# Performance work log

Measured on AMD Instinct MI355X. Metric: run time of the kernel, lower is better.

## Reference

```python
import jax, jax.numpy as jnp
import numpy as np

N, E, D, H, L = 100000, 800000, 64, 2, 2
C = D  # out_channels per head
NEG_SLOPE = 0.2


def setup_inputs() -> dict:
    key = jax.random.key(0)
    ks = jax.random.split(key, 10)
    x = jax.random.normal(ks[0], (N, D), dtype=jnp.float32)
    # random edges with no self loops (PyG GATv2 removes then re-adds self loops)
    src = jax.random.randint(ks[1], (E,), 0, N, dtype=jnp.int64)
    off = jax.random.randint(ks[2], (E,), 1, N, dtype=jnp.int64)
    dst = (src + off) % N
    edges_connectivity = jnp.stack([src, dst], axis=0)
    s = 1.0 / np.sqrt(D)
    Wl = jax.random.normal(ks[3], (L, D, H * C), dtype=jnp.float32) * s
    bl = jnp.zeros((L, H * C), dtype=jnp.float32)
    Wr = jax.random.normal(ks[4], (L, D, H * C), dtype=jnp.float32) * s
    br = jnp.zeros((L, H * C), dtype=jnp.float32)
    att = jax.random.normal(ks[5], (L, H, C), dtype=jnp.float32) * s
    bias = jnp.zeros((L, C), dtype=jnp.float32)
    return {"embeded_nodes_features": x, "edges_connectivity": edges_connectivity,
            "Wl": Wl, "bl": bl, "Wr": Wr, "br": br, "att": att, "bias": bias}


def _gatv2_layer(x, src, dst, Wl, bl, Wr, br, att, bias):
    # x: [N, D]; src/dst: [E'] (self loops already appended)
    xl = (x @ Wl + bl).reshape(N, H, C)
    xr = (x @ Wr + br).reshape(N, H, C)
    z = xl[src] + xr[dst]                                  # [E', H, C]
    e = jnp.einsum('ehc,hc->eh', jax.nn.leaky_relu(z, NEG_SLOPE), att)
    m = jax.ops.segment_max(e, dst, num_segments=N)        # [N, H]
    a = jnp.exp(e - m[dst])
    denom = jax.ops.segment_sum(a, dst, num_segments=N)    # [N, H]
    alpha = a / (denom[dst] + 1e-16)
    out = jax.ops.segment_sum(alpha[:, :, None] * xl[src], dst, num_segments=N)
    return out.mean(axis=1) + bias                         # concat=False -> mean over heads


def reference(embeded_nodes_features, edges_connectivity, Wl, bl, Wr, br, att, bias):
    loop = jnp.arange(N, dtype=edges_connectivity.dtype)
    src = jnp.concatenate([edges_connectivity[0], loop])
    dst = jnp.concatenate([edges_connectivity[1], loop])
    x = embeded_nodes_features  # dropout p=0 -> no-op
    for i in range(L):
        x = _gatv2_layer(x, src, dst, Wl[i], bl[i], Wr[i], br[i], att[i], bias[i])
        if i < L - 1:
            x = jax.nn.gelu(x)
    return x
```

## Files before the change

### kernel.cpp

```cpp
#include <hip/hip_runtime.h>
#include <math.h>

#define N_NODES 100000
#define N_EDGES 800000
#define D_IN    64
#define HC      128
#define CAP     48

#define GEMM_BLOCKS 1563
#define FUSED_BLOCKS (3 * GEMM_BLOCKS)

typedef short bf16x8 __attribute__((ext_vector_type(8)));
typedef float f32x4  __attribute__((ext_vector_type(4)));

__device__ __forceinline__ float gelu_f(float x) {
    float x3 = x * x * x;
    float y  = 0.7978845608028654f * (x + 0.044715f * x3);
    float t = 1.0f - 2.0f / (__expf(2.0f * y) + 1.0f);
    return 0.5f * x * (1.0f + t);
}

__device__ __forceinline__ float red16(float x) {
    x += __int_as_float(__builtin_amdgcn_mov_dpp(__float_as_int(x), 0x128, 0xF, 0xF, true));
    x += __int_as_float(__builtin_amdgcn_mov_dpp(__float_as_int(x), 0x124, 0xF, 0xF, true));
    x += __int_as_float(__builtin_amdgcn_mov_dpp(__float_as_int(x), 0x122, 0xF, 0xF, true));
    x += __int_as_float(__builtin_amdgcn_mov_dpp(__float_as_int(x), 0x121, 0xF, 0xF, true));
    return x;
}

__device__ __forceinline__ void bf16split(float x, unsigned short& h, unsigned short& l) {
    unsigned b  = __float_as_uint(x);
    unsigned hb = (b + 0x7FFFu + ((b >> 16) & 1u)) & 0xFFFF0000u;
    h = (unsigned short)(hb >> 16);
    float lo = x - __uint_as_float(hb);
    unsigned c = __float_as_uint(lo);
    l = (unsigned short)((c + 0x7FFFu + ((c >> 16) & 1u)) >> 16);
}

__global__ __launch_bounds__(256) void wprep_kernel(
    const float* __restrict__ Wl, const float* __restrict__ Wr,
    unsigned short* __restrict__ WBh, unsigned short* __restrict__ WBlo) {
    int g = blockIdx.x * 256 + threadIdx.x;
    int layer = g >> 14;
    int rem   = g & 16383;
    int col   = rem >> 6;
    int k     = rem & 63;
    const float* W = (col < 128) ? Wl : Wr;
    float x = W[layer * 8192 + k * HC + (col & 127)];
    unsigned short h, l;
    bf16split(x, h, l);
    WBh[g] = h; WBlo[g] = l;
}

__global__ __launch_bounds__(256, 3) void gemm_scatter_kernel(
    const float* __restrict__ X,
    const unsigned short* __restrict__ WBh, const unsigned short* __restrict__ WBlo,
    const float* __restrict__ bl, const float* __restrict__ br,
    float* __restrict__ XL, float* __restrict__ XR,
    const int* __restrict__ edges, int* __restrict__ cnt, int* __restrict__ tbl,
    int fused) {
    __shared__ unsigned short XH[64 * 64];
    __shared__ unsigned short XLo[64 * 64];

    const int t = threadIdx.x;
    int gid;
    if (fused) {
        const int g = blockIdx.x / 3, r = blockIdx.x % 3;
        if (r != 2) {
            const int e = (2 * g + r) * 256 + t;
            if (e < N_EDGES) {
                int s = edges[e];
                int d = edges[N_EDGES + e];
                int slot = atomicAdd(&cnt[d], 1);
                if (slot < CAP) tbl[d * CAP + slot] = s;
            }
            return;
        }
        gid = g;
    } else {
        gid = blockIdx.x;
    }
    const int n0 = gid * 64;

    #pragma unroll
    for (int p = 0; p < 4; ++p) {
        int f   = p * 256 + t;
        int row = f >> 4, q = f & 15;
        int gn  = n0 + row;
        float4 v = make_float4(0.0f, 0.0f, 0.0f, 0.0f);
        if (gn < N_NODES) v = *(const float4*)(X + (size_t)gn * D_IN + 4 * q);
        ushort4 h, l;
        bf16split(v.x, h.x, l.x); bf16split(v.y, h.y, l.y);
        bf16split(v.z, h.z, l.z); bf16split(v.w, h.w, l.w);
        int off = row * 64 + ((((q >> 1) ^ (row & 7))) << 3) + ((q & 1) << 2);
        *(ushort4*)&XH[off]  = h;
        *(ushort4*)&XLo[off] = l;
    }
    __syncthreads();

    const int lane = t & 63;
    const int w    = __builtin_amdgcn_readfirstlane(t >> 6);
    float* __restrict__ OUT = (w < 2) ? XL : XR;
    const float* __restrict__ bp = (w < 2) ? bl : br;
    const int cbase = (w & 1) * 64;
    const int lc    = lane & 15;
    const int lq    = lane >> 4;

    f32x4 acc[4][4];
    #pragma unroll
    for (int nt = 0; nt < 4; ++nt) {
        float bv = bp[cbase + nt * 16 + lc];
        #pragma unroll
        for (int mt = 0; mt < 4; ++mt)
            acc[mt][nt] = (f32x4){bv, bv, bv, bv};
    }

    #pragma unroll
    for (int kh = 0; kh < 2; ++kh) {
        bf16x8 Bh[4], Bl[4];
        #pragma unroll
        for (int nt = 0; nt < 4; ++nt) {
            int colg = w * 64 + nt * 16 + lc;
            int a = colg * 64 + kh * 32 + (lq << 3);
            Bh[nt] = *(const bf16x8*)(WBh + a);
            Bl[nt] = *(const bf16x8*)(WBlo + a);
        }
        #pragma unroll
        for (int mt = 0; mt < 4; ++mt) {
            int row = mt * 16 + lc;
            int aoff = row * 64 + ((((kh << 2) + lq) ^ (row & 7)) << 3);
            bf16x8 Ah = *(const bf16x8*)(XH + aoff);
            bf16x8 Al = *(const bf16x8*)(XLo + aoff);
            #pragma unroll
            for (int nt = 0; nt < 4; ++nt)
                acc[mt][nt] = __builtin_amdgcn_mfma_f32_16x16x32_bf16(Ah, Bh[nt], acc[mt][nt], 0, 0, 0);
            #pragma unroll
            for (int nt = 0; nt < 4; ++nt)
                acc[mt][nt] = __builtin_amdgcn_mfma_f32_16x16x32_bf16(Al, Bh[nt], acc[mt][nt], 0, 0, 0);
            #pragma unroll
            for (int nt = 0; nt < 4; ++nt)
                acc[mt][nt] = __builtin_amdgcn_mfma_f32_16x16x32_bf16(Ah, Bl[nt], acc[mt][nt], 0, 0, 0);
        }
    }

    #pragma unroll
    for (int mt = 0; mt < 4; ++mt) {
        int nbase = n0 + mt * 16 + (lq << 2);
        #pragma unroll
        for (int r = 0; r < 4; ++r) {
            int n = nbase + r;
            if (n < N_NODES) {
                float* o = OUT + (size_t)n * HC + cbase + lc;
                #pragma unroll
                for (int nt = 0; nt < 4; ++nt)
                    o[nt * 16] = acc[mt][nt][r];
            }
        }
    }
}

__global__ __launch_bounds__(256) void aggregate_kernel(
    const float* __restrict__ XL, const float* __restrict__ XR,
    const int* __restrict__ cnt, const int* __restrict__ tbl,
    const float* __restrict__ att, const float* __restrict__ bias,
    float* __restrict__ Y, int applyGelu) {
    const int wv   = (blockIdx.x * blockDim.x + threadIdx.x) >> 6;
    const int lane = threadIdx.x & 63;
    const int v    = 2 * wv + (lane >> 5);
    if (v >= N_NODES) return;
    const int li = lane & 15;
    const int hc = ((lane >> 4) & 1) * 64 + 4 * li;
    const int selbase = lane & 32;

    const float4 araw = *(const float4*)(att + hc);
    float4 a06, a04;
    a06.x = araw.x * 0.865617024f; a06.y = araw.y * 0.865617024f;
    a06.z = araw.z * 0.865617024f; a06.w = araw.w * 0.865617024f;
    a04.x = araw.x * 0.577078016f; a04.y = araw.y * 0.577078016f;
    a04.z = araw.z * 0.577078016f; a04.w = araw.w * 0.577078016f;
    const float4 xr4 = *(const float4*)(XR + (size_t)v * HC + hc);
    const float4 xl4 = *(const float4*)(XL + (size_t)v * HC + hc);

#define SCORE4(Z0, Z1, Z2, Z3, OUT)                                          \
    {                                                                        \
        float pa = (Z0) * a06.x;                                             \
        float pb = fabsf(Z0) * a04.x;                                        \
        pa = fmaf((Z1), a06.y, pa); pb = fmaf(fabsf(Z1), a04.y, pb);         \
        pa = fmaf((Z2), a06.z, pa); pb = fmaf(fabsf(Z2), a04.z, pb);         \
        pa = fmaf((Z3), a06.w, pa); pb = fmaf(fabsf(Z3), a04.w, pb);         \
        OUT = pa + pb;                                                       \
    }

    float z0 = xl4.x + xr4.x, z1 = xl4.y + xr4.y;
    float z2 = xl4.z + xr4.z, z3 = xl4.w + xr4.w;
    float p;
    SCORE4(z0, z1, z2, z3, p)
    const float m0 = red16(p);

    float s = 1.0f;
    float ax = xl4.x, ay = xl4.y, az = xl4.z, aw = xl4.w;

    int deg = cnt[v];
    if (deg > CAP) deg = CAP;
    const int slot = lane & 31;
    int u_l = (slot < deg) ? tbl[v * CAP + slot] : 0;

    int dmax = deg;
    { int d2 = __shfl_xor(deg, 32); dmax = d2 > dmax ? d2 : dmax; }

    const float* __restrict__ XLh = XL + hc;

    float4 x0 = make_float4(0,0,0,0), x1 = x0, x2 = x0;
    if (dmax > 0) { int u = __shfl(u_l, 0 + selbase); x0 = *(const float4*)(XLh + (size_t)u * HC); }
    if (dmax > 1) { int u = __shfl(u_l, 1 + selbase); x1 = *(const float4*)(XLh + (size_t)u * HC); }
    if (dmax > 2) { int u = __shfl(u_l, 2 + selbase); x2 = *(const float4*)(XLh + (size_t)u * HC); }

    for (int i = 0; i < dmax; ++i) {
        float4 xc = x0; x0 = x1; x1 = x2;
        int pf = i + 3;
        if (pf < dmax) {
            int u = (pf < 32) ? __shfl(u_l, pf + selbase) : tbl[v * CAP + pf];
            x2 = *(const float4*)(XLh + (size_t)u * HC);
        }
        z0 = xc.x + xr4.x; z1 = xc.y + xr4.y;
        z2 = xc.z + xr4.z; z3 = xc.w + xr4.w;
        SCORE4(z0, z1, z2, z3, p)
        p = red16(p);
        if (i >= deg) p = -1e30f;
        float w = exp2f(p - m0);
        s += w;
        ax = fmaf(w, xc.x, ax); ay = fmaf(w, xc.y, ay);
        az = fmaf(w, xc.z, az); aw = fmaf(w, xc.w, aw);
    }
#undef SCORE4

    float inv = 1.0f / (s + 1e-16f);
    ax *= inv; ay *= inv; az *= inv; aw *= inv;

    ax += __shfl_xor(ax, 16); ay += __shfl_xor(ay, 16);
    az += __shfl_xor(az, 16); aw += __shfl_xor(aw, 16);
    ax *= 0.5f; ay *= 0.5f; az *= 0.5f; aw *= 0.5f;

    if ((lane & 31) < 16) {
        const float4 b4 = *(const float4*)(bias + 4 * li);
        ax += b4.x; ay += b4.y; az += b4.z; aw += b4.w;
        if (applyGelu) { ax = gelu_f(ax); ay = gelu_f(ay); az = gelu_f(az); aw = gelu_f(aw); }
        *(float4*)(Y + (size_t)v * 64 + 4 * li) = make_float4(ax, ay, az, aw);
    }
}

extern "C" void kernel_launch(void* const* d_in, const int* in_sizes, int n_in,
                              void* d_out, int out_size, void* d_ws, size_t ws_size,
                              hipStream_t stream) {
    const float* X     = (const float*)d_in[0];
    const int*   edges = (const int*)d_in[1];
    const float* Wl    = (const float*)d_in[2];
    const float* bl    = (const float*)d_in[3];
    const float* Wr    = (const float*)d_in[4];
    const float* br    = (const float*)d_in[5];
    const float* att   = (const float*)d_in[6];
    const float* bias  = (const float*)d_in[7];

    char* ws = (char*)d_ws;
    float* XLb = (float*)ws;
    float* XRb = (float*)(ws + (size_t)N_NODES * HC * 4);
    float* Yb  = (float*)(ws + (size_t)N_NODES * HC * 8);
    int*   cnt = (int*)(ws + (size_t)N_NODES * HC * 8 + (size_t)N_NODES * 64 * 4);
    int*   tbl = cnt + N_NODES;
    unsigned short* WBh  = (unsigned short*)(tbl + (size_t)N_NODES * CAP);
    unsigned short* WBlo = WBh + 32768;

    hipMemsetAsync(cnt, 0, N_NODES * sizeof(int), stream);
    wprep_kernel<<<128, 256, 0, stream>>>(Wl, Wr, WBh, WBlo);

    const int agg_grid = ((N_NODES + 1) / 2 * 64 + 255) / 256;

    gemm_scatter_kernel<<<FUSED_BLOCKS, 256, 0, stream>>>(
        X, WBh, WBlo, bl, br, XLb, XRb, edges, cnt, tbl, 1);
    aggregate_kernel<<<agg_grid, 256, 0, stream>>>(XLb, XRb, cnt, tbl, att, bias, Yb, 1);
    gemm_scatter_kernel<<<GEMM_BLOCKS, 256, 0, stream>>>(
        Yb, WBh + 16384, WBlo + 16384, bl + 128, br + 128, XLb, XRb, edges, cnt, tbl, 0);
    aggregate_kernel<<<agg_grid, 256, 0, stream>>>(XLb, XRb, cnt, tbl, att + 128, bias + 64,
                                                   (float*)d_out, 0);
}
```

Before: 331.3 us.

## Stage GEMM output through LDS for coalesced float4 stores and pre-swizzle weights

The GEMM epilogue now writes accumulators into a shared-memory buffer that aliases the input tiles, then each wave writes whole rows with coalesced float4 stores to XL/XR instead of scattered scalar stores. The weight prep kernel lays out bf16 weights in per-lane fragment order so each lane loads B fragments contiguously. Launch bounds raise the occupancy target from 3 to 4 blocks per SIMD group. The extra syncthreads and LDS round trip add latency, and the higher occupancy target may force register spilling.

Measured after the change: 308.8 us. 6.8% less time.

```diff
diff --git a/kernel.cpp b/kernel.cpp
--- a/kernel.cpp
+++ b/kernel.cpp
@@ -43,8 +43,14 @@
     int g = blockIdx.x * 256 + threadIdx.x;
     int layer = g >> 14;
     int rem   = g & 16383;
-    int col   = rem >> 6;
-    int k     = rem & 63;
+    int j    = rem & 7;
+    int idx  = rem >> 3;
+    int lane = idx & 63;
+    int kh   = (idx >> 6) & 1;
+    int nt   = (idx >> 7) & 3;
+    int w    = (idx >> 9) & 3;
+    int col  = w * 64 + nt * 16 + (lane & 15);
+    int k    = kh * 32 + (lane >> 4) * 8 + j;
     const float* W = (col < 128) ? Wl : Wr;
     float x = W[layer * 8192 + k * HC + (col & 127)];
     unsigned short h, l;
@@ -52,15 +58,17 @@
     WBh[g] = h; WBlo[g] = l;
 }
 
-__global__ __launch_bounds__(256, 3) void gemm_scatter_kernel(
+__global__ __launch_bounds__(256, 4) void gemm_scatter_kernel(
     const float* __restrict__ X,
     const unsigned short* __restrict__ WBh, const unsigned short* __restrict__ WBlo,
     const float* __restrict__ bl, const float* __restrict__ br,
     float* __restrict__ XL, float* __restrict__ XR,
     const int* __restrict__ edges, int* __restrict__ cnt, int* __restrict__ tbl,
     int fused) {
-    __shared__ unsigned short XH[64 * 64];
-    __shared__ unsigned short XLo[64 * 64];
+    __shared__ union SMem {
+        struct { unsigned short XH[64 * 64]; unsigned short XLo[64 * 64]; } st;
+        float CS[32 * 268];
+    } sm;
 
     const int t = threadIdx.x;
     int gid;
@@ -93,14 +101,13 @@
         bf16split(v.x, h.x, l.x); bf16split(v.y, h.y, l.y);
         bf16split(v.z, h.z, l.z); bf16split(v.w, h.w, l.w);
         int off = row * 64 + ((((q >> 1) ^ (row & 7))) << 3) + ((q & 1) << 2);
-        *(ushort4*)&XH[off]  = h;
-        *(ushort4*)&XLo[off] = l;
+        *(ushort4*)&sm.st.XH[off]  = h;
+        *(ushort4*)&sm.st.XLo[off] = l;
     }
     __syncthreads();
 
     const int lane = t & 63;
     const int w    = __builtin_amdgcn_readfirstlane(t >> 6);
-    float* __restrict__ OUT = (w < 2) ? XL : XR;
     const float* __restrict__ bp = (w < 2) ? bl : br;
     const int cbase = (w & 1) * 64;
     const int lc    = lane & 15;
@@ -120,8 +127,7 @@
         bf16x8 Bh[4], Bl[4];
         #pragma unroll
         for (int nt = 0; nt < 4; ++nt) {
-            int colg = w * 64 + nt * 16 + lc;
-            int a = colg * 64 + kh * 32 + (lq << 3);
+            int a = (((w * 4 + nt) * 2 + kh) * 64 + lane) * 8;
             Bh[nt] = *(const bf16x8*)(WBh + a);
             Bl[nt] = *(const bf16x8*)(WBlo + a);
         }
@@ -129,8 +135,8 @@
         for (int mt = 0; mt < 4; ++mt) {
             int row = mt * 16 + lc;
             int aoff = row * 64 + ((((kh << 2) + lq) ^ (row & 7)) << 3);
-            bf16x8 Ah = *(const bf16x8*)(XH + aoff);
-            bf16x8 Al = *(const bf16x8*)(XLo + aoff);
+            bf16x8 Ah = *(const bf16x8*)(sm.st.XH + aoff);
+            bf16x8 Al = *(const bf16x8*)(sm.st.XLo + aoff);
             #pragma unroll
             for (int nt = 0; nt < 4; ++nt)
                 acc[mt][nt] = __builtin_amdgcn_mfma_f32_16x16x32_bf16(Ah, Bh[nt], acc[mt][nt], 0, 0, 0);
@@ -144,16 +150,27 @@
     }
 
     #pragma unroll
-    for (int mt = 0; mt < 4; ++mt) {
-        int nbase = n0 + mt * 16 + (lq << 2);
-        #pragma unroll
-        for (int r = 0; r < 4; ++r) {
-            int n = nbase + r;
+    for (int c = 0; c < 2; ++c) {
+        __syncthreads();
+        #pragma unroll
+        for (int mt2 = 0; mt2 < 2; ++mt2) {
+            int mt = 2 * c + mt2;
+            #pragma unroll
+            for (int nt = 0; nt < 4; ++nt)
+                #pragma unroll
+                for (int r = 0; r < 4; ++r)
+                    sm.CS[(mt2 * 16 + (lq << 2) + r) * 268 + w * 64 + nt * 16 + lc]
+                        = acc[mt][nt][r];
+        }
+        __syncthreads();
+        #pragma unroll
+        for (int i = 0; i < 8; ++i) {
+            int lr = i * 4 + w;
+            int n  = n0 + c * 32 + lr;
             if (n < N_NODES) {
-                float* o = OUT + (size_t)n * HC + cbase + lc;
-                #pragma unroll
-                for (int nt = 0; nt < 4; ++nt)
-                    o[nt * 16] = acc[mt][nt][r];
+                float4 v4 = *(const float4*)&sm.CS[lr * 268 + 4 * lane];
+                float* o = ((lane < 32) ? XL : XR) + (size_t)n * HC + (lane & 31) * 4;
+                *(float4*)o = v4;
             }
         }
     }
```
